# Kernel tuning notes

Hardware: AMD Instinct MI355X
Metric: run time of the kernel (lower is better)

The kernel has to match this reference:

```python
import jax, jax.numpy as jnp
import numpy as np

N, D_PHY, D_BOND, VOC = 512, 4, 128, 1024


def setup_inputs() -> dict:
    rng = np.random.default_rng(0)

    def cplx(shape, scale=1.0):
        return ((rng.standard_normal(shape) + 1j * rng.standard_normal(shape)) * scale).astype(np.complex64)

    A = cplx((VOC, D_PHY, D_PHY))                      # raw embedding params (QR applied in forward, as in torch M property)
    B0 = cplx((D_PHY, 1, D_BOND), 1.0 / np.sqrt(D_BOND))
    Bm = cplx((N - 2, D_PHY * D_BOND, D_BOND))
    Bm = np.linalg.qr(Bm)[0].reshape(N - 2, D_PHY, D_BOND, D_BOND).astype(np.complex64)  # left-isometric, as set_left_param
    Bl = cplx((D_PHY * D_BOND, 1))
    Bl = np.linalg.qr(Bl)[0].reshape(D_PHY, D_BOND, 1).astype(np.complex64)
    tokens = rng.integers(0, VOC, size=(N,))
    return {
        'a_re': jnp.asarray(A.real), 'a_im': jnp.asarray(A.imag),
        'b0_re': jnp.asarray(B0.real), 'b0_im': jnp.asarray(B0.imag),
        'bm_re': jnp.asarray(Bm.real), 'bm_im': jnp.asarray(Bm.imag),
        'bl_re': jnp.asarray(Bl.real), 'bl_im': jnp.asarray(Bl.imag),
        'tokens': jnp.asarray(tokens, dtype=jnp.int32),
    }


def _site(S, B, Mi):
    # S: (l, l') running density-like state; B: (p, l, r); Mi: (p, q) measurement op.
    # Equivalent to contracting torch's zipped = einsum(conj(B)[p,l,r], M[p,q], B[q,l',r'] -> [l,r,r',l'])
    # with the running state, but fused to avoid the (l,r,r',l') intermediate.
    t = jnp.einsum('ab,qbc->qac', S, B)      # (q, l, r')
    t = jnp.einsum('pq,qac->pac', Mi, t)     # (p, l, r')
    return jnp.einsum('plr,plc->rc', B.conj(), t)  # (r, r')


def reference(a_re, a_im, b0_re, b0_im, bm_re, bm_im, bl_re, bl_im, tokens):
    A = a_re + 1j * a_im                                  # (v, d, d)
    d = A.shape[-1]
    Aq = jnp.linalg.qr(A.reshape(-1, d))[0].reshape(A.shape)
    M = jnp.einsum('vij,vik->vjk', Aq.conj(), Aq)         # (v, d, d) POVM-like ops
    Ms = M[tokens]                                        # (n, d, d)

    B0 = b0_re + 1j * b0_im                               # (d, 1, D)
    Bm = bm_re + 1j * bm_im                               # (n-2, d, D, D)
    Bl = bl_re + 1j * bl_im                               # (d, D, 1)

    S = jnp.ones((1, 1), dtype=A.dtype)
    S = _site(S, B0, Ms[0])                               # (D, D)

    def step(S, xs):
        B, Mi = xs
        return _site(S, B, Mi), None

    S, _ = jax.lax.scan(step, S, (Bm, Ms[1:-1]))
    S = _site(S, Bl, Ms[-1])                              # (1, 1)
    return S.reshape(-1)                                  # complex64, shape (1,), as torch out.view(-1)
```

## Files before the change

### kernel.cpp

```cpp
#include <hip/hip_runtime.h>
#include <hip/hip_bf16.h>


__device__ __forceinline__ float2 cfma(float2 a, float2 b, float2 acc) {
    acc.x = fmaf(a.x, b.x, fmaf(-a.y, b.y, acc.x));
    acc.y = fmaf(a.x, b.y, fmaf( a.y, b.x, acc.y));
    return acc;
}
__device__ __forceinline__ float2 cfmac(float2 a, float2 b, float2 acc) {
    acc.x = fmaf(a.x, b.x, fmaf( a.y, b.y, acc.x));
    acc.y = fmaf(a.x, b.y, fmaf(-a.y, b.x, acc.y));
    return acc;
}

__device__ __forceinline__ float2 ld_coh(const float2* p) {
    union { unsigned long long u; float2 f; } cv;
    cv.u = __hip_atomic_load((const unsigned long long*)p,
                             __ATOMIC_RELAXED, __HIP_MEMORY_SCOPE_AGENT);
    return cv.f;
}
__device__ __forceinline__ void st_coh(float2* p, float2 x) {
    union { unsigned long long u; float2 f; } cv;
    cv.f = x;
    __hip_atomic_store((unsigned long long*)p, cv.u,
                       __ATOMIC_RELAXED, __HIP_MEMORY_SCOPE_AGENT);
}

__device__ __forceinline__ double2 d2mul(double2 a, double2 b) {
    return make_double2(a.x*b.x - a.y*b.y, a.x*b.y + a.y*b.x);
}
__device__ __forceinline__ double2 d2conj(double2 a) { return make_double2(a.x, -a.y); }
__device__ __forceinline__ double2 d2add(double2 a, double2 b) {
    return make_double2(a.x + b.x, a.y + b.y);
}
__device__ __forceinline__ double2 d2sub(double2 a, double2 b) {
    return make_double2(a.x - b.x, a.y - b.y);
}

__device__ __forceinline__ void lds_barrier() {
    asm volatile("s_waitcnt lgkmcnt(0)" ::: "memory");
    __builtin_amdgcn_s_barrier();
    __builtin_amdgcn_sched_barrier(0);
}

__device__ void redN(double2* v, int n, double2 (*redm)[4]) {
    for (int off = 32; off; off >>= 1) {
        for (int d = 0; d < n; ++d) {
            v[d].x += __shfl_down(v[d].x, off, 64);
            v[d].y += __shfl_down(v[d].y, off, 64);
        }
    }
    const int wid = threadIdx.x >> 6, lane = threadIdx.x & 63;
    __syncthreads();
    if (lane == 0)
        for (int d = 0; d < n; ++d) redm[wid][d] = v[d];
    __syncthreads();
    for (int d = 0; d < n; ++d) {
        double2 s = make_double2(0.0, 0.0);
        for (int w = 0; w < 9; ++w) { s.x += redm[w][d].x; s.y += redm[w][d].y; }
        v[d] = s;
    }
}

__device__ __forceinline__ float2 m_entry(const float* __restrict__ a_re,
                                          const float* __restrict__ a_im,
                                          int v, int m, const float2* Wl)
{
    const int j = m >> 2, k = m & 3;
    float2 Arow[4][4];
    #pragma unroll
    for (int i = 0; i < 4; ++i) {
        float4 re = *(const float4*)(a_re + v*16 + i*4);
        float4 im = *(const float4*)(a_im + v*16 + i*4);
        Arow[i][0] = make_float2(re.x, im.x);
        Arow[i][1] = make_float2(re.y, im.y);
        Arow[i][2] = make_float2(re.z, im.z);
        Arow[i][3] = make_float2(re.w, im.w);
    }
    float2 acc = make_float2(0.f, 0.f);
    #pragma unroll
    for (int i = 0; i < 4; ++i) {
        float2 yj = make_float2(0.f, 0.f), yk = yj;
        #pragma unroll
        for (int q = 0; q < 4; ++q) {
            yj = cfma(Arow[i][q], Wl[q*4 + j], yj);
            yk = cfma(Arow[i][q], Wl[q*4 + k], yk);
        }
        acc = cfmac(yj, yk, acc);
    }
    return acc;
}

__global__ __launch_bounds__(512) void zero_cnt(unsigned int* __restrict__ cnt)
{
    cnt[threadIdx.x] = 0u;
}

#define NWG 128u
__device__ __forceinline__ bool site_barrier(unsigned int* addr,
                                             unsigned* nzw, int* live_lds, int tid)
{
    asm volatile("s_waitcnt lgkmcnt(0)" ::: "memory");
    if (tid < 128) asm volatile("s_waitcnt vmcnt(0)" ::: "memory");
    __builtin_amdgcn_s_barrier();
    __builtin_amdgcn_sched_barrier(0);
    if (tid == 0) {
        unsigned add = 1u | ((nzw[0] | nzw[1]) ? 0x10000u : 0u);
        __hip_atomic_fetch_add(addr, add, __ATOMIC_RELAXED, __HIP_MEMORY_SCOPE_AGENT);
        unsigned v;
        for (;;) {
            v = __hip_atomic_load(addr, __ATOMIC_RELAXED, __HIP_MEMORY_SCOPE_AGENT);
            if ((v & 0xffffu) >= NWG) break;
            __builtin_amdgcn_s_sleep(1);
        }
        *live_lds = (int)(v >> 16);
    }
    asm volatile("s_waitcnt lgkmcnt(0)" ::: "memory");
    __builtin_amdgcn_s_barrier();
    __builtin_amdgcn_sched_barrier(0);
    return *live_lds != 0;
}

__global__ __launch_bounds__(576, 3) void scan_kernel(
    const float* __restrict__ a_re,  const float* __restrict__ a_im,
    const float* __restrict__ b0_re, const float* __restrict__ b0_im,
    const float* __restrict__ bm_re, const float* __restrict__ bm_im,
    const float* __restrict__ bl_re, const float* __restrict__ bl_im,
    const int*  __restrict__ tokens,
    float2* SbufA, float2* SbufB,
    unsigned int* cnt, float* out, int out_size)
{
    const int tid = threadIdx.x;
    const int bid = blockIdx.x;
    const int c   = ((bid & 7) << 4) | (bid >> 3);
    const int i16 = bid >> 3;

    __shared__ float2 Clds[4][128];
    __shared__ float4 Upart4[8][256];
    __shared__ float4 U4[256];
    __shared__ float4 P16_4[16][64];
    __shared__ float2 Bpre[2][4][128];
    __shared__ float2 fred[16];
    __shared__ double2 redm[9][4];
    __shared__ float2 Wlds[16];
    __shared__ float2 MtLds[2][16];
    __shared__ unsigned nzw[2];
    __shared__ int live_lds;

    const int a = tid & 127;
    const int h = tid >> 7;

    float2* Sread = SbufA;
    float2* Swrite = SbufB;
    bool dead = false;
    float warmacc = 0.f;
    float wm0 = 0.f, wm1 = 0.f, wm2 = 0.f, wm3 = 0.f;

    if (tid < 512) {
        const float4* t0r = (const float4*)bm_re + i16*1024;
        const float4* t0i = (const float4*)bm_im + i16*1024;
        #pragma unroll
        for (int k = 0; k < 2; ++k) {
            float4 x0 = t0r[tid + k*512],          y0 = t0i[tid + k*512];
            float4 x1 = t0r[16384 + tid + k*512],  y1 = t0i[16384 + tid + k*512];
            warmacc += x0.x+x0.y+x0.z+x0.w + y0.x+y0.y+y0.z+y0.w
                     + x1.x+x1.y+x1.z+x1.w + y1.x+y1.y+y1.z+y1.w;
        }
    }

    double2 gp[10];
    #pragma unroll
    for (int e = 0; e < 10; ++e) gp[e] = make_double2(0.0, 0.0);
    if (tid < 512) {
        for (int rr = 0; rr < 8; ++rr) {
            const int r = tid * 8 + rr;
            float4 fre = *(const float4*)(a_re + r*4);
            float4 fim = *(const float4*)(a_im + r*4);
            double r0 = fre.x, r1 = fre.y, r2 = fre.z, r3 = fre.w;
            double i0 = fim.x, i1 = fim.y, i2 = fim.z, i3 = fim.w;
#define GACC(e, rj, ij, rk, ik) \
            gp[e].x += rj*rk + ij*ik; gp[e].y += rj*ik - ij*rk;
            GACC(0, r0, i0, r0, i0)  GACC(1, r0, i0, r1, i1)
            GACC(2, r0, i0, r2, i2)  GACC(3, r0, i0, r3, i3)
            GACC(4, r1, i1, r1, i1)  GACC(5, r1, i1, r2, i2)
            GACC(6, r1, i1, r3, i3)  GACC(7, r2, i2, r2, i2)
            GACC(8, r2, i2, r3, i3)  GACC(9, r3, i3, r3, i3)
#undef GACC
        }
    }
    redN(gp + 0, 4, redm);
    redN(gp + 4, 4, redm);
    redN(gp + 8, 2, redm);

    double2 G4[4][4];
    G4[0][0]=gp[0]; G4[0][1]=gp[1]; G4[0][2]=gp[2]; G4[0][3]=gp[3];
    G4[1][1]=gp[4]; G4[1][2]=gp[5]; G4[1][3]=gp[6];
    G4[2][2]=gp[7]; G4[2][3]=gp[8]; G4[3][3]=gp[9];
    G4[1][0]=d2conj(gp[1]); G4[2][0]=d2conj(gp[2]); G4[3][0]=d2conj(gp[3]);
    G4[2][1]=d2conj(gp[5]); G4[3][1]=d2conj(gp[6]); G4[3][2]=d2conj(gp[8]);
    G4[0][0].y=0.0; G4[1][1].y=0.0; G4[2][2].y=0.0; G4[3][3].y=0.0;

    {
        double2 T[4][4];
        #pragma unroll
        for (int i = 0; i < 4; ++i)
            #pragma unroll
            for (int j = 0; j < 4; ++j)
                T[i][j] = make_double2((double)a_re[i*4+j], (double)a_im[i*4+j]);

        double dsgn[4];
        #pragma unroll
        for (int k = 0; k < 4; ++k) {
            double ssum = 0.0;
            #pragma unroll
            for (int i = 0; i < 4; ++i)
                if (i <= k) ssum += T[i][k].x*T[i][k].x + T[i][k].y*T[i][k].y;
            double xn = G4[k][k].x - ssum; if (xn < 0.0) xn = 0.0;
            double ar = T[k][k].x, ai = T[k][k].y;
            double nrm = sqrt(ar*ar + ai*ai + xn);
            double beta = (ar >= 0.0) ? -nrm : nrm;
            dsgn[k] = (beta >= 0.0) ? 1.0 : -1.0;
            double2 tau = make_double2((beta - ar)/beta, -ai/beta);
            double dr = ar - beta, di = ai;
            double dd = dr*dr + di*di;
            double2 s = make_double2(dr/dd, -di/dd);
            double2 w[4];
            #pragma unroll
            for (int j = 0; j < 4; ++j) if (j > k) {
                double2 acc = G4[k][j];
                #pragma unroll
                for (int i = 0; i < 4; ++i)
                    if (i <= k) acc = d2sub(acc, d2mul(d2conj(T[i][k]), T[i][j]));
                w[j] = d2add(T[k][j], d2mul(d2conj(s), acc));
            }
            #pragma unroll
            for (int j = 0; j < 4; ++j) if (j > k) {
                double2 tw = d2mul(tau, w[j]);
                T[k][j] = d2sub(T[k][j], tw);
                #pragma unroll
                for (int i = 0; i < 4; ++i)
                    if (i > k) T[i][j] = d2sub(T[i][j], d2mul(tw, d2mul(s, T[i][k])));
            }
            T[k][k] = make_double2(beta, 0.0);
            #pragma unroll
            for (int i = 0; i < 4; ++i)
                if (i > k) T[i][k] = make_double2(0.0, 0.0);
        }

        double2 R[4][4];
        #pragma unroll
        for (int k = 0; k < 4; ++k) {
            double dk = G4[k][k].x;
            #pragma unroll
            for (int i = 0; i < 4; ++i)
                if (i < k) dk -= R[i][k].x*R[i][k].x + R[i][k].y*R[i][k].y;
            if (dk < 1e-30) dk = 1e-30;
            double rkk = sqrt(dk);
            R[k][k] = make_double2(rkk, 0.0);
            #pragma unroll
            for (int j = 0; j < 4; ++j) if (j > k) {
                double2 acc = G4[k][j];
                #pragma unroll
                for (int i = 0; i < 4; ++i)
                    if (i < k) acc = d2sub(acc, d2mul(d2conj(R[i][k]), R[i][j]));
                R[k][j] = make_double2(acc.x/rkk, acc.y/rkk);
            }
        }
        double2 X[4][4];
        #pragma unroll
        for (int j = 0; j < 4; ++j) {
            #pragma unroll
            for (int i = 0; i < 4; ++i) X[i][j] = make_double2(0.0, 0.0);
            X[j][j] = make_double2(1.0 / R[j][j].x, 0.0);
            #pragma unroll
            for (int ii = 0; ii < 3; ++ii) {
                const int i = j - 1 - ii;
                if (i >= 0) {
                    double2 acc = make_double2(0.0, 0.0);
                    #pragma unroll
                    for (int m2 = 0; m2 < 4; ++m2)
                        if (m2 > i && m2 <= j) acc = d2add(acc, d2mul(R[i][m2], X[m2][j]));
                    X[i][j] = make_double2(-acc.x / R[i][i].x, -acc.y / R[i][i].x);
                }
            }
        }
        if (tid == 0) {
            #pragma unroll
            for (int q = 0; q < 4; ++q)
                #pragma unroll
                for (int j = 0; j < 4; ++j)
                    Wlds[q*4 + j] = make_float2((float)(X[q][j].x * dsgn[j]),
                                                (float)(X[q][j].y * dsgn[j]));
        }
    }
    __syncthreads();

    if (tid < 32) {
        const int which = tid >> 4, m = tid & 15;
        MtLds[which][m] = m_entry(a_re, a_im, tokens[which], m, Wlds);
    }
    if (tid < 512) {
        Bpre[1][h][a] = make_float2(bm_re[(h*128 + a)*128 + c],
                                    bm_im[(h*128 + a)*128 + c]);
    }
    __syncthreads();

    if (tid < 128) {
        const int r = a;
        float2 brr[4], bcc[4];
        for (int p = 0; p < 4; ++p) {
            brr[p] = make_float2(b0_re[p*128 + r], b0_im[p*128 + r]);
            bcc[p] = make_float2(b0_re[p*128 + c], b0_im[p*128 + c]);
        }
        float2 acc = make_float2(0.f, 0.f);
        for (int p = 0; p < 4; ++p) {
            float2 tp = make_float2(0.f, 0.f);
            for (int q = 0; q < 4; ++q) tp = cfma(MtLds[0][p*4 + q], bcc[q], tp);
            acc = cfmac(brr[p], tp, acc);
        }
        st_coh(&SbufA[c*128 + r], acc);
        int nz = (acc.x != 0.f) || (acc.y != 0.f);
        unsigned long long m = __ballot(nz);
        if ((tid & 63) == 0) nzw[tid >> 6] = (m != 0ULL) ? 1u : 0u;
    }

    if (!site_barrier(&cnt[0], nzw, &live_lds, tid)) dead = true;

    if (!dead) {
        for (int t = 1; t <= 510; ++t) {
            const int cur = t & 1, nxt = cur ^ 1;
            const float* br = bm_re + (size_t)(t - 1) * 65536;
            const float* bi = bm_im + (size_t)(t - 1) * 65536;

            float2 bp[8];
            float2 macc = make_float2(0.f, 0.f);
            int j = 0;
            if (tid >= 512) {
                j = tid - 512;
                warmacc += wm0 + wm1 + wm2 + wm3;
                if (t < 510) {
                    const float* br2 = bm_re + (size_t)t * 65536;
                    const float* bi2 = bm_im + (size_t)t * 65536;
                    #pragma unroll
                    for (int e = 0; e < 8; ++e) {
                        const int idx = j + e*64, q = idx >> 7, a2i = idx & 127;
                        bp[e] = make_float2(br2[(q*128 + a2i)*128 + c],
                                            bi2[(q*128 + a2i)*128 + c]);
                    }
                }
                if (j < 16) macc = m_entry(a_re, a_im, tokens[t+1], j, Wlds);
                if (t < 509) {
                    const float* wr = bm_re + (size_t)(t+1)*65536 + i16*4096;
                    const float* wi = bm_im + (size_t)(t+1)*65536 + i16*4096;
                    wm0 = wr[j*32];  wm1 = wr[2048 + j*32];
                    wm2 = wi[j*32];  wm3 = wi[2048 + j*32];
                } else { wm0 = wm1 = wm2 = wm3 = 0.f; }
            }

            if (tid < 512) {
                float2 acc = make_float2(0.f, 0.f);
                #pragma unroll
                for (int q = 0; q < 4; ++q)
                    acc = cfma(MtLds[cur][h*4 + q], Bpre[cur][q][a], acc);
                Clds[h][a] = acc;
            }
            lds_barrier();

            if (tid < 512) {
                const int sub = tid >> 6, a2 = tid & 63;
                float2 u00 = make_float2(0,0), u01 = u00, u02 = u00, u03 = u00;
                float2 u10 = u00, u11 = u00, u12 = u00, u13 = u00;
                {
                    const float2* _b0 = Sread + (sub*16)*128 + 2*a2;
                    const float2* _b1 = _b0 + 512;
                    const float2* _b2 = _b0 + 1024;
                    const float2* _b3 = _b0 + 1536;
                    float4 t0,t1,t2,t3,t4,t5,t6,t7,t8,t9,t10,t11,t12,t13,t14,t15;
                    asm volatile(
                      "global_load_dwordx4 %0, %16, off sc0 sc1\n\t"
                      "global_load_dwordx4 %1, %16, off offset:1024 sc0 sc1\n\t"
                      "global_load_dwordx4 %2, %16, off offset:2048 sc0 sc1\n\t"
                      "global_load_dwordx4 %3, %16, off offset:3072 sc0 sc1\n\t"
                      "global_load_dwordx4 %4, %17, off sc0 sc1\n\t"
                      "global_load_dwordx4 %5, %17, off offset:1024 sc0 sc1\n\t"
                      "global_load_dwordx4 %6, %17, off offset:2048 sc0 sc1\n\t"
                      "global_load_dwordx4 %7, %17, off offset:3072 sc0 sc1\n\t"
                      "global_load_dwordx4 %8, %18, off sc0 sc1\n\t"
                      "global_load_dwordx4 %9, %18, off offset:1024 sc0 sc1\n\t"
                      "global_load_dwordx4 %10, %18, off offset:2048 sc0 sc1\n\t"
                      "global_load_dwordx4 %11, %18, off offset:3072 sc0 sc1\n\t"
                      "global_load_dwordx4 %12, %19, off sc0 sc1\n\t"
                      "global_load_dwordx4 %13, %19, off offset:1024 sc0 sc1\n\t"
                      "global_load_dwordx4 %14, %19, off offset:2048 sc0 sc1\n\t"
                      "global_load_dwordx4 %15, %19, off offset:3072 sc0 sc1\n\t"
                      "s_waitcnt vmcnt(0)"
                      : "=&v"(t0), "=&v"(t1), "=&v"(t2), "=&v"(t3),
                        "=&v"(t4), "=&v"(t5), "=&v"(t6), "=&v"(t7),
                        "=&v"(t8), "=&v"(t9), "=&v"(t10), "=&v"(t11),
                        "=&v"(t12), "=&v"(t13), "=&v"(t14), "=&v"(t15)
                      : "v"(_b0), "v"(_b1), "v"(_b2), "v"(_b3));
                    float4 tt[16] = {t0,t1,t2,t3,t4,t5,t6,t7,
                                     t8,t9,t10,t11,t12,t13,t14,t15};
                    #pragma unroll
                    for (int e = 0; e < 16; ++e) {
                        const int b = sub*16 + e;
                        float2 slo = make_float2(tt[e].x, tt[e].y);
                        float2 shi = make_float2(tt[e].z, tt[e].w);
                        float2 c0 = Clds[0][b], c1 = Clds[1][b];
                        float2 c2 = Clds[2][b], c3 = Clds[3][b];
                        u00 = cfma(slo, c0, u00);  u10 = cfma(shi, c0, u10);
                        u01 = cfma(slo, c1, u01);  u11 = cfma(shi, c1, u11);
                        u02 = cfma(slo, c2, u02);  u12 = cfma(shi, c2, u12);
                        u03 = cfma(slo, c3, u03);  u13 = cfma(shi, c3, u13);
                    }
                }
                Upart4[sub][0*64 + a2] = make_float4(u00.x,u00.y,u10.x,u10.y);
                Upart4[sub][1*64 + a2] = make_float4(u01.x,u01.y,u11.x,u11.y);
                Upart4[sub][2*64 + a2] = make_float4(u02.x,u02.y,u12.x,u12.y);
                Upart4[sub][3*64 + a2] = make_float4(u03.x,u03.y,u13.x,u13.y);
            }
            lds_barrier();
            if (tid < 256) {
                float4 s = Upart4[0][tid];
                #pragma unroll
                for (int w = 1; w < 8; ++w) {
                    float4 x = Upart4[w][tid];
                    s.x += x.x; s.y += x.y; s.z += x.z; s.w += x.w;
                }
                U4[tid] = s;
            }
            lds_barrier();

            if (tid < 512) {
                const int pg = tid >> 5, r4 = tid & 31;
                const int p = pg >> 2, abase = (pg & 3) * 32;
                const int pabase = pg * 32;
                const float4* br4 = (const float4*)br;
                const float4* bi4 = (const float4*)bi;
                float2 o0 = make_float2(0,0), o1 = o0, o2 = o0, o3 = o0;
                #pragma unroll 4
                for (int k = 0; k < 32; k += 2) {
                    float4 u2 = U4[p*64 + ((abase + k) >> 1)];
                    float2 Ua = make_float2(u2.x, u2.y);
                    float2 Ub = make_float2(u2.z, u2.w);
                    float4 ra = br4[(pabase + k)*32 + r4];
                    float4 ia = bi4[(pabase + k)*32 + r4];
                    float4 rb = br4[(pabase + k + 1)*32 + r4];
                    float4 ib = bi4[(pabase + k + 1)*32 + r4];
                    o0 = cfmac(make_float2(ra.x, ia.x), Ua, o0);
                    o1 = cfmac(make_float2(ra.y, ia.y), Ua, o1);
                    o2 = cfmac(make_float2(ra.z, ia.z), Ua, o2);
                    o3 = cfmac(make_float2(ra.w, ia.w), Ua, o3);
                    o0 = cfmac(make_float2(rb.x, ib.x), Ub, o0);
                    o1 = cfmac(make_float2(rb.y, ib.y), Ub, o1);
                    o2 = cfmac(make_float2(rb.z, ib.z), Ub, o2);
                    o3 = cfmac(make_float2(rb.w, ib.w), Ub, o3);
                }
                P16_4[pg][r4]      = make_float4(o0.x,o0.y,o1.x,o1.y);
                P16_4[pg][32 + r4] = make_float4(o2.x,o2.y,o3.x,o3.y);
            }
            lds_barrier();
            if (tid < 128) {
                const int r = a;
                const int m = r & 3, q = r >> 2;
                const int pidx = (m < 2) ? (2*q + m) : (64 + 2*q + (m - 2));
                const float2* Prow = (const float2*)(&P16_4[0][0]);
                float2 fin = make_float2(0,0);
                #pragma unroll
                for (int w = 0; w < 16; ++w) {
                    float2 x = Prow[w*128 + pidx];
                    fin.x += x.x; fin.y += x.y;
                }
                st_coh(&Swrite[c * 128 + r], fin);
                int nz = (fin.x != 0.f) || (fin.y != 0.f);
                unsigned long long m2 = __ballot(nz);
                if ((tid & 63) == 0) nzw[tid >> 6] = (m2 != 0ULL) ? 1u : 0u;
            }

            if (tid >= 512) {
                if (t < 510) {
                    #pragma unroll
                    for (int e = 0; e < 8; ++e) {
                        const int idx = j + e*64, q = idx >> 7, a2i = idx & 127;
                        Bpre[nxt][q][a2i] = bp[e];
                    }
                }
                if (j < 16) MtLds[nxt][j] = macc;
            }

            if (!site_barrier(&cnt[t], nzw, &live_lds, tid)) { dead = true; break; }
            float2* tmp = Sread; Sread = Swrite; Swrite = tmp;
        }
    }
    warmacc += wm0 + wm1 + wm2 + wm3;

    if (out_size < 0) out[2] = warmacc;

    if (dead) {
        if (bid == 0 && tid == 0) {
            out[0] = 0.f;
            if (out_size > 1) out[1] = 0.f;
        }
        return;
    }
    if (bid != 0) return;

    if (tid < 512) {
        float2 acc = make_float2(0,0);
        for (int b = 0; b < 128; ++b) {
            float2 s = ld_coh(&Sread[b * 128 + a]);
            float2 bl = make_float2(bl_re[h*128 + b], bl_im[h*128 + b]);
            acc = cfma(s, bl, acc);
        }
        Clds[h][a] = acc;
    }
    __syncthreads();
    float2 tot = make_float2(0,0);
    if (tid < 512) {
        float2 tp = make_float2(0,0);
        for (int q = 0; q < 4; ++q) tp = cfma(MtLds[1][h*4 + q], Clds[q][a], tp);
        float2 blv = make_float2(bl_re[h*128 + a], bl_im[h*128 + a]);
        tot = cfmac(blv, tp, make_float2(0,0));
    }
    for (int off = 32; off; off >>= 1) {
        tot.x += __shfl_down(tot.x, off, 64);
        tot.y += __shfl_down(tot.y, off, 64);
    }
    if ((tid & 63) == 0) fred[tid >> 6] = tot;
    __syncthreads();
    if (tid == 0) {
        float2 s = make_float2(0,0);
        for (int w = 0; w < 9; ++w) { s.x += fred[w].x; s.y += fred[w].y; }
        out[0] = s.x;
        if (out_size > 1) out[1] = s.y;
    }
}

extern "C" void kernel_launch(void* const* d_in, const int* in_sizes, int n_in,
                              void* d_out, int out_size, void* d_ws, size_t ws_size,
                              hipStream_t stream)
{
    const float* a_re  = (const float*)d_in[0];
    const float* a_im  = (const float*)d_in[1];
    const float* b0_re = (const float*)d_in[2];
    const float* b0_im = (const float*)d_in[3];
    const float* bm_re = (const float*)d_in[4];
    const float* bm_im = (const float*)d_in[5];
    const float* bl_re = (const float*)d_in[6];
    const float* bl_im = (const float*)d_in[7];
    const int*  tokens = (const int*)d_in[8];

    char* ws = (char*)d_ws;
    float2* S0   = (float2*)(ws + 196608);
    float2* S1b  = (float2*)(ws + 327680);
    unsigned int* cnt = (unsigned int*)(ws + 458752);

    zero_cnt<<<dim3(1), dim3(512), 0, stream>>>(cnt);

    float* outf = (float*)d_out;
    int osz = out_size;
    void* args[] = {
        (void*)&a_re, (void*)&a_im, (void*)&b0_re, (void*)&b0_im,
        (void*)&bm_re, (void*)&bm_im, (void*)&bl_re, (void*)&bl_im,
        (void*)&tokens,
        (void*)&S0, (void*)&S1b, (void*)&cnt, (void*)&outf, (void*)&osz
    };
    hipLaunchCooperativeKernel((const void*)scan_kernel, dim3(128), dim3(576),
                               args, 0, stream);
}
```

Baseline: 226.6 us.

## Compute QR whitening matrix once in prep kernel instead of per workgroup

The Gram-matrix reduction over the embedding table and the 4x4 QR/triangular-inverse that builds the whitening matrix move out of the cooperative scan kernel. They now run once in a single-block prep kernel, which also zeroes the barrier counters. Each of the 128 scan workgroups then loads the 16 results from global memory rather than recomputing them redundantly. The per-site 16-load batch is also split into two 8-load batches, which lowers register pressure at the cost of an extra vmcnt wait.

```diff
diff --git a/kernel.cpp b/kernel.cpp
--- a/kernel.cpp
+++ b/kernel.cpp
@@ -43,7 +43,36 @@
     __builtin_amdgcn_sched_barrier(0);
 }
 
-__device__ void redN(double2* v, int n, double2 (*redm)[4]) {
+__device__ __forceinline__ float2 m_entry(const float* __restrict__ a_re,
+                                          const float* __restrict__ a_im,
+                                          int v, int m, const float2* Wl)
+{
+    const int j = m >> 2, k = m & 3;
+    float2 Arow[4][4];
+    #pragma unroll
+    for (int i = 0; i < 4; ++i) {
+        float4 re = *(const float4*)(a_re + v*16 + i*4);
+        float4 im = *(const float4*)(a_im + v*16 + i*4);
+        Arow[i][0] = make_float2(re.x, im.x);
+        Arow[i][1] = make_float2(re.y, im.y);
+        Arow[i][2] = make_float2(re.z, im.z);
+        Arow[i][3] = make_float2(re.w, im.w);
+    }
+    float2 acc = make_float2(0.f, 0.f);
+    #pragma unroll
+    for (int i = 0; i < 4; ++i) {
+        float2 yj = make_float2(0.f, 0.f), yk = yj;
+        #pragma unroll
+        for (int q = 0; q < 4; ++q) {
+            yj = cfma(Arow[i][q], Wl[q*4 + j], yj);
+            yk = cfma(Arow[i][q], Wl[q*4 + k], yk);
+        }
+        acc = cfmac(yj, yk, acc);
+    }
+    return acc;
+}
+
+__device__ void redN8(double2* v, int n, double2 (*redm)[4]) {
     for (int off = 32; off; off >>= 1) {
         for (int d = 0; d < n; ++d) {
             v[d].x += __shfl_down(v[d].x, off, 64);
@@ -57,43 +86,141 @@
     __syncthreads();
     for (int d = 0; d < n; ++d) {
         double2 s = make_double2(0.0, 0.0);
-        for (int w = 0; w < 9; ++w) { s.x += redm[w][d].x; s.y += redm[w][d].y; }
+        for (int w = 0; w < 8; ++w) { s.x += redm[w][d].x; s.y += redm[w][d].y; }
         v[d] = s;
     }
 }
 
-__device__ __forceinline__ float2 m_entry(const float* __restrict__ a_re,
-                                          const float* __restrict__ a_im,
-                                          int v, int m, const float2* Wl)
+__global__ __launch_bounds__(512) void prep_kernel(const float* __restrict__ a_re,
+                                                   const float* __restrict__ a_im,
+                                                   float2* __restrict__ Wout,
+                                                   unsigned int* __restrict__ cnt)
 {
-    const int j = m >> 2, k = m & 3;
-    float2 Arow[4][4];
-    #pragma unroll
-    for (int i = 0; i < 4; ++i) {
-        float4 re = *(const float4*)(a_re + v*16 + i*4);
-        float4 im = *(const float4*)(a_im + v*16 + i*4);
-        Arow[i][0] = make_float2(re.x, im.x);
-        Arow[i][1] = make_float2(re.y, im.y);
-        Arow[i][2] = make_float2(re.z, im.z);
-        Arow[i][3] = make_float2(re.w, im.w);
-    }
-    float2 acc = make_float2(0.f, 0.f);
-    #pragma unroll
-    for (int i = 0; i < 4; ++i) {
-        float2 yj = make_float2(0.f, 0.f), yk = yj;
-        #pragma unroll
-        for (int q = 0; q < 4; ++q) {
-            yj = cfma(Arow[i][q], Wl[q*4 + j], yj);
-            yk = cfma(Arow[i][q], Wl[q*4 + k], yk);
-        }
-        acc = cfmac(yj, yk, acc);
-    }
-    return acc;
-}
-
-__global__ __launch_bounds__(512) void zero_cnt(unsigned int* __restrict__ cnt)
-{
-    cnt[threadIdx.x] = 0u;
+    const int t = threadIdx.x;
+    cnt[t] = 0u;
+    __shared__ double2 redm[8][4];
+
+    double2 gp[10];
+    #pragma unroll
+    for (int e = 0; e < 10; ++e) gp[e] = make_double2(0.0, 0.0);
+    for (int rr = 0; rr < 8; ++rr) {
+        const int r = t * 8 + rr;
+        float4 fre = *(const float4*)(a_re + r*4);
+        float4 fim = *(const float4*)(a_im + r*4);
+        double r0 = fre.x, r1 = fre.y, r2 = fre.z, r3 = fre.w;
+        double i0 = fim.x, i1 = fim.y, i2 = fim.z, i3 = fim.w;
+#define GACC(e, rj, ij, rk, ik) \
+        gp[e].x += rj*rk + ij*ik; gp[e].y += rj*ik - ij*rk;
+        GACC(0, r0, i0, r0, i0)  GACC(1, r0, i0, r1, i1)
+        GACC(2, r0, i0, r2, i2)  GACC(3, r0, i0, r3, i3)
+        GACC(4, r1, i1, r1, i1)  GACC(5, r1, i1, r2, i2)
+        GACC(6, r1, i1, r3, i3)  GACC(7, r2, i2, r2, i2)
+        GACC(8, r2, i2, r3, i3)  GACC(9, r3, i3, r3, i3)
+#undef GACC
+    }
+    redN8(gp + 0, 4, redm);
+    redN8(gp + 4, 4, redm);
+    redN8(gp + 8, 2, redm);
+
+    if (t != 0) return;
+
+    double2 G4[4][4];
+    G4[0][0]=gp[0]; G4[0][1]=gp[1]; G4[0][2]=gp[2]; G4[0][3]=gp[3];
+    G4[1][1]=gp[4]; G4[1][2]=gp[5]; G4[1][3]=gp[6];
+    G4[2][2]=gp[7]; G4[2][3]=gp[8]; G4[3][3]=gp[9];
+    G4[1][0]=d2conj(gp[1]); G4[2][0]=d2conj(gp[2]); G4[3][0]=d2conj(gp[3]);
+    G4[2][1]=d2conj(gp[5]); G4[3][1]=d2conj(gp[6]); G4[3][2]=d2conj(gp[8]);
+    G4[0][0].y=0.0; G4[1][1].y=0.0; G4[2][2].y=0.0; G4[3][3].y=0.0;
+
+    double2 T[4][4];
+    #pragma unroll
+    for (int i = 0; i < 4; ++i)
+        #pragma unroll
+        for (int j = 0; j < 4; ++j)
+            T[i][j] = make_double2((double)a_re[i*4+j], (double)a_im[i*4+j]);
+
+    double dsgn[4];
+    #pragma unroll
+    for (int k = 0; k < 4; ++k) {
+        double ssum = 0.0;
+        #pragma unroll
+        for (int i = 0; i < 4; ++i)
+            if (i <= k) ssum += T[i][k].x*T[i][k].x + T[i][k].y*T[i][k].y;
+        double xn = G4[k][k].x - ssum; if (xn < 0.0) xn = 0.0;
+        double ar = T[k][k].x, ai = T[k][k].y;
+        double nrm = sqrt(ar*ar + ai*ai + xn);
+        double beta = (ar >= 0.0) ? -nrm : nrm;
+        dsgn[k] = (beta >= 0.0) ? 1.0 : -1.0;
+        double2 tau = make_double2((beta - ar)/beta, -ai/beta);
+        double dr = ar - beta, di = ai;
+        double dd = dr*dr + di*di;
+        double2 s = make_double2(dr/dd, -di/dd);
+        double2 w[4];
+        #pragma unroll
+        for (int j = 0; j < 4; ++j) if (j > k) {
+            double2 acc = G4[k][j];
+            #pragma unroll
+            for (int i = 0; i < 4; ++i)
+                if (i <= k) acc = d2sub(acc, d2mul(d2conj(T[i][k]), T[i][j]));
+            w[j] = d2add(T[k][j], d2mul(d2conj(s), acc));
+        }
+        #pragma unroll
+        for (int j = 0; j < 4; ++j) if (j > k) {
+            double2 tw = d2mul(tau, w[j]);
+            T[k][j] = d2sub(T[k][j], tw);
+            #pragma unroll
+            for (int i = 0; i < 4; ++i)
+                if (i > k) T[i][j] = d2sub(T[i][j], d2mul(tw, d2mul(s, T[i][k])));
+        }
+        T[k][k] = make_double2(beta, 0.0);
+        #pragma unroll
+        for (int i = 0; i < 4; ++i)
+            if (i > k) T[i][k] = make_double2(0.0, 0.0);
+    }
+
+    double2 R[4][4];
+    #pragma unroll
+    for (int k = 0; k < 4; ++k) {
+        double dk = G4[k][k].x;
+        #pragma unroll
+        for (int i = 0; i < 4; ++i)
+            if (i < k) dk -= R[i][k].x*R[i][k].x + R[i][k].y*R[i][k].y;
+        if (dk < 1e-30) dk = 1e-30;
+        double rkk = sqrt(dk);
+        R[k][k] = make_double2(rkk, 0.0);
+        #pragma unroll
+        for (int j = 0; j < 4; ++j) if (j > k) {
+            double2 acc = G4[k][j];
+            #pragma unroll
+            for (int i = 0; i < 4; ++i)
+                if (i < k) acc = d2sub(acc, d2mul(d2conj(R[i][k]), R[i][j]));
+            R[k][j] = make_double2(acc.x/rkk, acc.y/rkk);
+        }
+    }
+    double2 X[4][4];
+    #pragma unroll
+    for (int j = 0; j < 4; ++j) {
+        #pragma unroll
+        for (int i = 0; i < 4; ++i) X[i][j] = make_double2(0.0, 0.0);
+        X[j][j] = make_double2(1.0 / R[j][j].x, 0.0);
+        #pragma unroll
+        for (int ii = 0; ii < 3; ++ii) {
+            const int i = j - 1 - ii;
+            if (i >= 0) {
+                double2 acc = make_double2(0.0, 0.0);
+                #pragma unroll
+                for (int m2 = 0; m2 < 4; ++m2)
+                    if (m2 > i && m2 <= j) acc = d2add(acc, d2mul(R[i][m2], X[m2][j]));
+                X[i][j] = make_double2(-acc.x / R[i][i].x, -acc.y / R[i][i].x);
+            }
+        }
+    }
+    #pragma unroll
+    for (int q = 0; q < 4; ++q)
+        #pragma unroll
+        for (int j = 0; j < 4; ++j)
+            Wout[q*4 + j] = make_float2((float)(X[q][j].x * dsgn[j]),
+                                        (float)(X[q][j].y * dsgn[j]));
 }
 
 #define NWG 128u
@@ -121,12 +248,43 @@
     return *live_lds != 0;
 }
 
+#define LD8X4_FMA(E0, PA, PB)                                                 \
+  {                                                                           \
+    float4 t0,t1,t2,t3,t4,t5,t6,t7;                                           \
+    asm volatile(                                                             \
+      "global_load_dwordx4 %0, %8, off sc0 sc1\n\t"                           \
+      "global_load_dwordx4 %1, %8, off offset:1024 sc0 sc1\n\t"               \
+      "global_load_dwordx4 %2, %8, off offset:2048 sc0 sc1\n\t"               \
+      "global_load_dwordx4 %3, %8, off offset:3072 sc0 sc1\n\t"               \
+      "global_load_dwordx4 %4, %9, off sc0 sc1\n\t"                           \
+      "global_load_dwordx4 %5, %9, off offset:1024 sc0 sc1\n\t"               \
+      "global_load_dwordx4 %6, %9, off offset:2048 sc0 sc1\n\t"               \
+      "global_load_dwordx4 %7, %9, off offset:3072 sc0 sc1\n\t"               \
+      "s_waitcnt vmcnt(0)"                                                    \
+      : "=&v"(t0), "=&v"(t1), "=&v"(t2), "=&v"(t3),                           \
+        "=&v"(t4), "=&v"(t5), "=&v"(t6), "=&v"(t7)                            \
+      : "v"(PA), "v"(PB));                                                    \
+    float4 tt[8] = {t0,t1,t2,t3,t4,t5,t6,t7};                                 \
+    _Pragma("unroll")                                                         \
+    for (int e = 0; e < 8; ++e) {                                             \
+        const int b = sub*16 + (E0) + e;                                      \
+        float2 slo = make_float2(tt[e].x, tt[e].y);                           \
+        float2 shi = make_float2(tt[e].z, tt[e].w);                           \
+        float2 c0 = Clds[0][b], c1 = Clds[1][b];                              \
+        float2 c2 = Clds[2][b], c3 = Clds[3][b];                              \
+        u00 = cfma(slo, c0, u00);  u10 = cfma(shi, c0, u10);                  \
+        u01 = cfma(slo, c1, u01);  u11 = cfma(shi, c1, u11);                  \
+        u02 = cfma(slo, c2, u02);  u12 = cfma(shi, c2, u12);                  \
+        u03 = cfma(slo, c3, u03);  u13 = cfma(shi, c3, u13);                  \
+    }                                                                         \
+  }
+
 __global__ __launch_bounds__(576, 3) void scan_kernel(
     const float* __restrict__ a_re,  const float* __restrict__ a_im,
     const float* __restrict__ b0_re, const float* __restrict__ b0_im,
     const float* __restrict__ bm_re, const float* __restrict__ bm_im,
     const float* __restrict__ bl_re, const float* __restrict__ bl_im,
-    const int*  __restrict__ tokens,
+    const int*  __restrict__ tokens, const float2* __restrict__ Wglob,
     float2* SbufA, float2* SbufB,
     unsigned int* cnt, float* out, int out_size)
 {
@@ -141,7 +299,6 @@
     __shared__ float4 P16_4[16][64];
     __shared__ float2 Bpre[2][4][128];
     __shared__ float2 fred[16];
-    __shared__ double2 redm[9][4];
     __shared__ float2 Wlds[16];
     __shared__ float2 MtLds[2][16];
     __shared__ unsigned nzw[2];
@@ -168,131 +325,7 @@
         }
     }
 
-    double2 gp[10];
-    #pragma unroll
-    for (int e = 0; e < 10; ++e) gp[e] = make_double2(0.0, 0.0);
-    if (tid < 512) {
-        for (int rr = 0; rr < 8; ++rr) {
-            const int r = tid * 8 + rr;
-            float4 fre = *(const float4*)(a_re + r*4);
-            float4 fim = *(const float4*)(a_im + r*4);
-            double r0 = fre.x, r1 = fre.y, r2 = fre.z, r3 = fre.w;
-            double i0 = fim.x, i1 = fim.y, i2 = fim.z, i3 = fim.w;
-#define GACC(e, rj, ij, rk, ik) \
-            gp[e].x += rj*rk + ij*ik; gp[e].y += rj*ik - ij*rk;
-            GACC(0, r0, i0, r0, i0)  GACC(1, r0, i0, r1, i1)
-            GACC(2, r0, i0, r2, i2)  GACC(3, r0, i0, r3, i3)
-            GACC(4, r1, i1, r1, i1)  GACC(5, r1, i1, r2, i2)
-            GACC(6, r1, i1, r3, i3)  GACC(7, r2, i2, r2, i2)
-            GACC(8, r2, i2, r3, i3)  GACC(9, r3, i3, r3, i3)
-#undef GACC
-        }
-    }
-    redN(gp + 0, 4, redm);
-    redN(gp + 4, 4, redm);
-    redN(gp + 8, 2, redm);
-
-    double2 G4[4][4];
-    G4[0][0]=gp[0]; G4[0][1]=gp[1]; G4[0][2]=gp[2]; G4[0][3]=gp[3];
-    G4[1][1]=gp[4]; G4[1][2]=gp[5]; G4[1][3]=gp[6];
-    G4[2][2]=gp[7]; G4[2][3]=gp[8]; G4[3][3]=gp[9];
-    G4[1][0]=d2conj(gp[1]); G4[2][0]=d2conj(gp[2]); G4[3][0]=d2conj(gp[3]);
-    G4[2][1]=d2conj(gp[5]); G4[3][1]=d2conj(gp[6]); G4[3][2]=d2conj(gp[8]);
-    G4[0][0].y=0.0; G4[1][1].y=0.0; G4[2][2].y=0.0; G4[3][3].y=0.0;
-
-    {
-        double2 T[4][4];
-        #pragma unroll
-        for (int i = 0; i < 4; ++i)
-            #pragma unroll
-            for (int j = 0; j < 4; ++j)
-                T[i][j] = make_double2((double)a_re[i*4+j], (double)a_im[i*4+j]);
-
-        double dsgn[4];
-        #pragma unroll
-        for (int k = 0; k < 4; ++k) {
-            double ssum = 0.0;
-            #pragma unroll
-            for (int i = 0; i < 4; ++i)
-                if (i <= k) ssum += T[i][k].x*T[i][k].x + T[i][k].y*T[i][k].y;
-            double xn = G4[k][k].x - ssum; if (xn < 0.0) xn = 0.0;
-            double ar = T[k][k].x, ai = T[k][k].y;
-            double nrm = sqrt(ar*ar + ai*ai + xn);
-            double beta = (ar >= 0.0) ? -nrm : nrm;
-            dsgn[k] = (beta >= 0.0) ? 1.0 : -1.0;
-            double2 tau = make_double2((beta - ar)/beta, -ai/beta);
-            double dr = ar - beta, di = ai;
-            double dd = dr*dr + di*di;
-            double2 s = make_double2(dr/dd, -di/dd);
-            double2 w[4];
-            #pragma unroll
-            for (int j = 0; j < 4; ++j) if (j > k) {
-                double2 acc = G4[k][j];
-                #pragma unroll
-                for (int i = 0; i < 4; ++i)
-                    if (i <= k) acc = d2sub(acc, d2mul(d2conj(T[i][k]), T[i][j]));
-                w[j] = d2add(T[k][j], d2mul(d2conj(s), acc));
-            }
-            #pragma unroll
-            for (int j = 0; j < 4; ++j) if (j > k) {
-                double2 tw = d2mul(tau, w[j]);
-                T[k][j] = d2sub(T[k][j], tw);
-                #pragma unroll
-                for (int i = 0; i < 4; ++i)
-                    if (i > k) T[i][j] = d2sub(T[i][j], d2mul(tw, d2mul(s, T[i][k])));
-            }
-            T[k][k] = make_double2(beta, 0.0);
-            #pragma unroll
-            for (int i = 0; i < 4; ++i)
-                if (i > k) T[i][k] = make_double2(0.0, 0.0);
-        }
-
-        double2 R[4][4];
-        #pragma unroll
-        for (int k = 0; k < 4; ++k) {
-            double dk = G4[k][k].x;
-            #pragma unroll
-            for (int i = 0; i < 4; ++i)
-                if (i < k) dk -= R[i][k].x*R[i][k].x + R[i][k].y*R[i][k].y;
-            if (dk < 1e-30) dk = 1e-30;
-            double rkk = sqrt(dk);
-            R[k][k] = make_double2(rkk, 0.0);
-            #pragma unroll
-            for (int j = 0; j < 4; ++j) if (j > k) {
-                double2 acc = G4[k][j];
-                #pragma unroll
-                for (int i = 0; i < 4; ++i)
-                    if (i < k) acc = d2sub(acc, d2mul(d2conj(R[i][k]), R[i][j]));
-                R[k][j] = make_double2(acc.x/rkk, acc.y/rkk);
-            }
-        }
-        double2 X[4][4];
-        #pragma unroll
-        for (int j = 0; j < 4; ++j) {
-            #pragma unroll
-            for (int i = 0; i < 4; ++i) X[i][j] = make_double2(0.0, 0.0);
-            X[j][j] = make_double2(1.0 / R[j][j].x, 0.0);
-            #pragma unroll
-            for (int ii = 0; ii < 3; ++ii) {
-                const int i = j - 1 - ii;
-                if (i >= 0) {
-                    double2 acc = make_double2(0.0, 0.0);
-                    #pragma unroll
-                    for (int m2 = 0; m2 < 4; ++m2)
-                        if (m2 > i && m2 <= j) acc = d2add(acc, d2mul(R[i][m2], X[m2][j]));
-                    X[i][j] = make_double2(-acc.x / R[i][i].x, -acc.y / R[i][i].x);
-                }
-            }
-        }
-        if (tid == 0) {
-            #pragma unroll
-            for (int q = 0; q < 4; ++q)
-                #pragma unroll
-                for (int j = 0; j < 4; ++j)
-                    Wlds[q*4 + j] = make_float2((float)(X[q][j].x * dsgn[j]),
-                                                (float)(X[q][j].y * dsgn[j]));
-        }
-    }
+    if (tid < 16) Wlds[tid] = Wglob[tid];
     __syncthreads();
 
     if (tid < 32) {
@@ -370,50 +403,12 @@
                 const int sub = tid >> 6, a2 = tid & 63;
                 float2 u00 = make_float2(0,0), u01 = u00, u02 = u00, u03 = u00;
                 float2 u10 = u00, u11 = u00, u12 = u00, u13 = u00;
-                {
-                    const float2* _b0 = Sread + (sub*16)*128 + 2*a2;
-                    const float2* _b1 = _b0 + 512;
-                    const float2* _b2 = _b0 + 1024;
-                    const float2* _b3 = _b0 + 1536;
-                    float4 t0,t1,t2,t3,t4,t5,t6,t7,t8,t9,t10,t11,t12,t13,t14,t15;
-                    asm volatile(
-                      "global_load_dwordx4 %0, %16, off sc0 sc1\n\t"
-                      "global_load_dwordx4 %1, %16, off offset:1024 sc0 sc1\n\t"
-                      "global_load_dwordx4 %2, %16, off offset:2048 sc0 sc1\n\t"
-                      "global_load_dwordx4 %3, %16, off offset:3072 sc0 sc1\n\t"
-                      "global_load_dwordx4 %4, %17, off sc0 sc1\n\t"
-                      "global_load_dwordx4 %5, %17, off offset:1024 sc0 sc1\n\t"
-                      "global_load_dwordx4 %6, %17, off offset:2048 sc0 sc1\n\t"
-                      "global_load_dwordx4 %7, %17, off offset:3072 sc0 sc1\n\t"
-                      "global_load_dwordx4 %8, %18, off sc0 sc1\n\t"
-                      "global_load_dwordx4 %9, %18, off offset:1024 sc0 sc1\n\t"
-                      "global_load_dwordx4 %10, %18, off offset:2048 sc0 sc1\n\t"
-                      "global_load_dwordx4 %11, %18, off offset:3072 sc0 sc1\n\t"
-                      "global_load_dwordx4 %12, %19, off sc0 sc1\n\t"
-                      "global_load_dwordx4 %13, %19, off offset:1024 sc0 sc1\n\t"
-                      "global_load_dwordx4 %14, %19, off offset:2048 sc0 sc1\n\t"
-                      "global_load_dwordx4 %15, %19, off offset:3072 sc0 sc1\n\t"
-                      "s_waitcnt vmcnt(0)"
-                      : "=&v"(t0), "=&v"(t1), "=&v"(t2), "=&v"(t3),
-                        "=&v"(t4), "=&v"(t5), "=&v"(t6), "=&v"(t7),
-                        "=&v"(t8), "=&v"(t9), "=&v"(t10), "=&v"(t11),
-                        "=&v"(t12), "=&v"(t13), "=&v"(t14), "=&v"(t15)
-                      : "v"(_b0), "v"(_b1), "v"(_b2), "v"(_b3));
-                    float4 tt[16] = {t0,t1,t2,t3,t4,t5,t6,t7,
-                                     t8,t9,t10,t11,t12,t13,t14,t15};
-                    #pragma unroll
-                    for (int e = 0; e < 16; ++e) {
-                        const int b = sub*16 + e;
-                        float2 slo = make_float2(tt[e].x, tt[e].y);
-                        float2 shi = make_float2(tt[e].z, tt[e].w);
-                        float2 c0 = Clds[0][b], c1 = Clds[1][b];
-                        float2 c2 = Clds[2][b], c3 = Clds[3][b];
-                        u00 = cfma(slo, c0, u00);  u10 = cfma(shi, c0, u10);
-                        u01 = cfma(slo, c1, u01);  u11 = cfma(shi, c1, u11);
-                        u02 = cfma(slo, c2, u02);  u12 = cfma(shi, c2, u12);
-                        u03 = cfma(slo, c3, u03);  u13 = cfma(shi, c3, u13);
-                    }
-                }
+                const float2* _b0 = Sread + (sub*16)*128 + 2*a2;
+                const float2* _b1 = _b0 + 512;
+                const float2* _b2 = _b0 + 1024;
+                const float2* _b3 = _b0 + 1536;
+                LD8X4_FMA(0, _b0, _b1)
+                LD8X4_FMA(8, _b2, _b3)
                 Upart4[sub][0*64 + a2] = make_float4(u00.x,u00.y,u10.x,u10.y);
                 Upart4[sub][1*64 + a2] = make_float4(u01.x,u01.y,u11.x,u11.y);
                 Upart4[sub][2*64 + a2] = make_float4(u02.x,u02.y,u12.x,u12.y);
@@ -554,15 +549,16 @@
     float2* S0   = (float2*)(ws + 196608);
     float2* S1b  = (float2*)(ws + 327680);
     unsigned int* cnt = (unsigned int*)(ws + 458752);
-
-    zero_cnt<<<dim3(1), dim3(512), 0, stream>>>(cnt);
+    float2* W    = (float2*)(ws + 460800);
+
+    prep_kernel<<<dim3(1), dim3(512), 0, stream>>>(a_re, a_im, W, cnt);
 
     float* outf = (float*)d_out;
     int osz = out_size;
     void* args[] = {
         (void*)&a_re, (void*)&a_im, (void*)&b0_re, (void*)&b0_im,
         (void*)&bm_re, (void*)&bm_im, (void*)&bl_re, (void*)&bl_im,
-        (void*)&tokens,
+        (void*)&tokens, (void*)&W,
         (void*)&S0, (void*)&S1b, (void*)&cnt, (void*)&outf, (void*)&osz
     };
     hipLaunchCooperativeKernel((const void*)scan_kernel, dim3(128), dim3(576),
```

Result: faster. 197.6 us (median of 2 runs) (-12.8%).
